# Kernel optimization log

Measured on AMD Instinct MI355X. Metric: run time of the kernel, lower is better.

The kernel has to match this reference:

```python
import jax, jax.numpy as jnp
import numpy as np

D_MODEL = 1024
D_K = 64
HEADS = 16


def setup_inputs() -> dict:
    key = jax.random.key(0)
    k = jax.random.split(key, 7)
    b, s = 4, 2048
    scale = 1.0 / np.sqrt(D_MODEL)
    return {
        "input_Q": jax.random.normal(k[0], (b, s, D_MODEL), jnp.float32),
        "input_K": jax.random.normal(k[1], (b, s, D_MODEL), jnp.float32),
        "input_V": jax.random.normal(k[2], (b, s, D_MODEL), jnp.float32),
        "W_Q": jax.random.normal(k[3], (D_MODEL, D_K * HEADS), jnp.float32) * scale,
        "W_K": jax.random.normal(k[4], (D_MODEL, D_K * HEADS), jnp.float32) * scale,
        "W_V": jax.random.normal(k[5], (D_MODEL, D_K * HEADS), jnp.float32) * scale,
        "W_O": jax.random.normal(k[6], (D_K * HEADS, D_MODEL), jnp.float32) * scale,
    }


def reference(input_Q, input_K, input_V, W_Q, W_K, W_V, W_O):
    b, s, _ = input_Q.shape
    # project and split heads: [b, s, h*d] -> [b, h, s, d]
    def split_heads(x):
        return x.reshape(b, -1, HEADS, D_K).transpose(0, 2, 1, 3)

    Q = split_heads(input_Q @ W_Q)
    K = split_heads(input_K @ W_K)
    V = split_heads(input_V @ W_V)

    scores = jnp.einsum("bhsd,bhtd->bhst", Q, K) / np.sqrt(D_K)  # [b,h,s,s]
    attn = jax.nn.softmax(scores, axis=-1)
    value = jnp.einsum("bhst,bhtd->bhsd", attn, V)  # [b,h,s,d]
    value = value.transpose(0, 2, 1, 3).reshape(b, s, HEADS * D_K)
    return value @ W_O
```

## Files before the change

kernel.cpp:

```cpp
#include <hip/hip_runtime.h>
#include <stdint.h>

#define DM 1024
#define HD 64
#define NH 16
#define SEQ 2048
#define NB 4

typedef __bf16 bf16x8 __attribute__((ext_vector_type(8)));
typedef __bf16 bf16x4 __attribute__((ext_vector_type(4)));
typedef float f32x4 __attribute__((ext_vector_type(4)));

#define EXP2F(x) __builtin_amdgcn_exp2f(x)

__device__ __forceinline__ float bf2f(uint16_t b) {
    uint32_t u = ((uint32_t)b) << 16;
    float f;
    __builtin_memcpy(&f, &u, 4);
    return f;
}
__device__ __forceinline__ uint16_t f2bf(float f) {
    uint32_t u;
    __builtin_memcpy(&u, &f, 4);
    u += 0x7fffu + ((u >> 16) & 1u);
    return (uint16_t)(u >> 16);
}

__device__ __forceinline__ void gll16(const void* g, void* l) {
    __builtin_amdgcn_global_load_lds(
        (const __attribute__((address_space(1))) void*)g,
        (__attribute__((address_space(3))) void*)l, 16, 0, 0);
}

__global__ __launch_bounds__(256) void cvt_f32_bf16(const float* __restrict__ in,
                                                    uint16_t* __restrict__ out) {
    const size_t i = (size_t)blockIdx.x * 256 + threadIdx.x;
    const float4* p = (const float4*)in + i * 2;
    const float4 a = p[0], b = p[1];
    uint16_t o[8] = {f2bf(a.x), f2bf(a.y), f2bf(a.z), f2bf(a.w),
                     f2bf(b.x), f2bf(b.y), f2bf(b.z), f2bf(b.w)};
    __builtin_memcpy(out + i * 8, o, 16);
}

__global__ void transpose_cvt4(const float* __restrict__ w0,
                               const float* __restrict__ w1,
                               const float* __restrict__ w2,
                               const float* __restrict__ w3,
                               uint16_t* __restrict__ o0,
                               uint16_t* __restrict__ o1,
                               uint16_t* __restrict__ o2,
                               uint16_t* __restrict__ o3) {
    __shared__ uint16_t t[32][33];
    const float* in;
    uint16_t* out;
    switch (blockIdx.z) {
        case 0: in = w0; out = o0; break;
        case 1: in = w1; out = o1; break;
        case 2: in = w2; out = o2; break;
        default: in = w3; out = o3; break;
    }
    const int bx = blockIdx.x * 32, by = blockIdx.y * 32;
    const int tx = threadIdx.x, ty = threadIdx.y;
#pragma unroll
    for (int i = ty; i < 32; i += 8)
        t[i][tx] = f2bf(in[(size_t)(by + i) * DM + bx + tx]);
    __syncthreads();
#pragma unroll
    for (int i = ty; i < 32; i += 8)
        out[(size_t)(bx + i) * DM + by + tx] = t[tx][i];
}

__global__ void transpose_bf16(const uint16_t* __restrict__ in,
                               uint16_t* __restrict__ out, int R, int C) {
    __shared__ uint16_t t[32][33];
    const int bx = blockIdx.x * 32, by = blockIdx.y * 32;
    const size_t zo = (size_t)blockIdx.z * R * C;
    in += zo; out += zo;
    const int tx = threadIdx.x, ty = threadIdx.y;
#pragma unroll
    for (int i = ty; i < 32; i += 8)
        t[i][tx] = in[(size_t)(by + i) * C + bx + tx];
    __syncthreads();
#pragma unroll
    for (int i = ty; i < 32; i += 8)
        out[(size_t)(bx + i) * R + by + tx] = t[tx][i];
}

template <typename OT>
__global__ __launch_bounds__(256) void gemm_bf16(
    const uint16_t* __restrict__ A, const uint16_t* __restrict__ Bt,
    OT* __restrict__ C, int M, int N, int K) {
    __shared__ uint16_t As[2][128 * 64];
    __shared__ uint16_t Bs[2][128 * 64];
    const int tid = threadIdx.x;
    const int wave = tid >> 6, lane = tid & 63;
    const int g = lane >> 4, l15 = lane & 15;
    const int m0 = blockIdx.y * 128, n0 = blockIdx.x * 128;
    const int wr = wave >> 1, wc = wave & 1;

    size_t aglob[4], bglob[4];
    int ldsOff[4];
#pragma unroll
    for (int i = 0; i < 4; i++) {
        const int c = wave * 4 + i;
        const int o = (c * 64 + lane) * 16;
        const int row = o >> 7, off = o & 127;
        const int soff = off ^ ((row & 7) << 4);
        aglob[i] = ((size_t)(m0 + row) * K << 1) + soff;
        bglob[i] = ((size_t)(n0 + row) * K << 1) + soff;
        ldsOff[i] = c * 1024;
    }

    f32x4 acc[4][4];
    const f32x4 z4 = {0.f, 0.f, 0.f, 0.f};
#pragma unroll
    for (int i = 0; i < 4; i++)
#pragma unroll
        for (int j = 0; j < 4; j++) acc[i][j] = z4;

#pragma unroll
    for (int i = 0; i < 4; i++) {
        gll16((const char*)A + aglob[i], (char*)As[0] + ldsOff[i]);
        gll16((const char*)Bt + bglob[i], (char*)Bs[0] + ldsOff[i]);
    }
#pragma unroll
    for (int i = 0; i < 4; i++) {
        gll16((const char*)A + aglob[i] + 128, (char*)As[1] + ldsOff[i]);
        gll16((const char*)Bt + bglob[i] + 128, (char*)Bs[1] + ldsOff[i]);
    }

    const int steps = K >> 6;
    for (int s = 0; s < steps; s++) {
        if (s + 1 < steps)
            asm volatile("s_waitcnt vmcnt(8)" ::: "memory");
        else
            asm volatile("s_waitcnt vmcnt(0)" ::: "memory");
        __builtin_amdgcn_sched_barrier(0);
        __builtin_amdgcn_s_barrier();
        __builtin_amdgcn_sched_barrier(0);

        const uint16_t* as = As[s & 1];
        const uint16_t* bs = Bs[s & 1];
#pragma unroll
        for (int ks = 0; ks < 2; ks++) {
            bf16x8 a[4], b[4];
#pragma unroll
            for (int mi = 0; mi < 4; mi++) {
                const int row = wr * 64 + mi * 16 + l15;
                a[mi] = *(const bf16x8*)((const char*)as + row * 128 +
                                         ((ks * 64 + g * 16) ^ ((row & 7) << 4)));
            }
#pragma unroll
            for (int ni = 0; ni < 4; ni++) {
                const int row = wc * 64 + ni * 16 + l15;
                b[ni] = *(const bf16x8*)((const char*)bs + row * 128 +
                                         ((ks * 64 + g * 16) ^ ((row & 7) << 4)));
            }
#pragma unroll
            for (int mi = 0; mi < 4; mi++)
#pragma unroll
                for (int ni = 0; ni < 4; ni++)
                    acc[mi][ni] = __builtin_amdgcn_mfma_f32_16x16x32_bf16(
                        a[mi], b[ni], acc[mi][ni], 0, 0, 0);
        }

        __builtin_amdgcn_sched_barrier(0);
        __builtin_amdgcn_s_barrier();
        __builtin_amdgcn_sched_barrier(0);

        if (s + 2 < steps) {
            const size_t kb = ((size_t)(s + 2) << 7);
#pragma unroll
            for (int i = 0; i < 4; i++) {
                gll16((const char*)A + aglob[i] + kb, (char*)As[s & 1] + ldsOff[i]);
                gll16((const char*)Bt + bglob[i] + kb, (char*)Bs[s & 1] + ldsOff[i]);
            }
        }
    }

#pragma unroll
    for (int mi = 0; mi < 4; mi++)
#pragma unroll
        for (int ni = 0; ni < 4; ni++) {
            const int row = m0 + wr * 64 + mi * 16 + g * 4;
            const int col = n0 + wc * 64 + ni * 16 + l15;
#pragma unroll
            for (int r = 0; r < 4; r++) {
                if constexpr (sizeof(OT) == 4)
                    C[(size_t)(row + r) * N + col] = acc[mi][ni][r];
                else
                    C[(size_t)(row + r) * N + col] = f2bf(acc[mi][ni][r]);
            }
        }
}

__global__ __launch_bounds__(256, 2) void attn_fwd(
    const uint16_t* __restrict__ Q, const uint16_t* __restrict__ Kb,
    const uint16_t* __restrict__ Vt, uint16_t* __restrict__ AO) {
    __shared__ uint16_t smem[6 * 4096];
    const int tid = threadIdx.x;
    const int wave = tid >> 6, lane = tid & 63;
    const int g = lane >> 4, l15 = lane & 15;
    const int qt = blockIdx.x, h = blockIdx.y, b = blockIdx.z;
    const int q0 = qt * 256 + wave * 64;
    const int NT = SEQ / 64;
    const float SM_BIAS = 12.0f;

    uint16_t* const KsBase = smem;
    uint16_t* const VsBase = smem + 3 * 4096;

    size_t kglob[2], vglob[2];
    int ldsOff[2];
#pragma unroll
    for (int i = 0; i < 2; i++) {
        const int c = wave * 2 + i;
        const int r3 = (lane >> 3) & 7;
        const int soff = ((lane & 7) << 4) ^ (r3 << 4);
        const int kappa = (((c >> 1) & 1) << 5) | ((c & 1) << 4) |
                          (((lane >> 5) & 1) << 3) | (((c >> 2) & 1) << 2) |
                          (r3 & 3);
        kglob[i] = (((size_t)(b * SEQ + kappa) * DM + h * HD) << 1) + soff;
        vglob[i] = (((size_t)(b * DM + h * HD + c * 8 + r3) * SEQ) << 1) + soff;
        ldsOff[i] = c * 1024;
    }

    const float QSCALE = 0.125f * 1.44269504088896f;
    bf16x8 qf[4][2];
#pragma unroll
    for (int qi = 0; qi < 4; qi++)
#pragma unroll
        for (int ks = 0; ks < 2; ks++) {
            const uint16_t* src = Q + (size_t)(b * SEQ + q0 + qi * 16 + l15) * DM +
                                  h * HD + ks * 32 + g * 8;
            uint16_t tmp[8], ov[8];
            __builtin_memcpy(tmp, src, 16);
#pragma unroll
            for (int j = 0; j < 8; j++) ov[j] = f2bf(bf2f(tmp[j]) * QSCALE);
            __builtin_memcpy(&qf[qi][ks], ov, 16);
        }

    f32x4 accO[4][4];
    const f32x4 z4 = {0.f, 0.f, 0.f, 0.f};
#pragma unroll
    for (int i = 0; i < 4; i++)
#pragma unroll
        for (int j = 0; j < 4; j++) accO[i][j] = z4;
    float l_run[4] = {0.f, 0.f, 0.f, 0.f};

#pragma unroll
    for (int i = 0; i < 2; i++) {
        gll16((const char*)Kb + kglob[i], (char*)KsBase + ldsOff[i]);
        gll16((const char*)Vt + vglob[i], (char*)VsBase + ldsOff[i]);
    }
    {
        const size_t kadv = (size_t)(64 * DM * 2);
        const size_t vadv = (size_t)(64 * 2);
#pragma unroll
        for (int i = 0; i < 2; i++) {
            gll16((const char*)Kb + kglob[i] + kadv, (char*)KsBase + 8192 + ldsOff[i]);
            gll16((const char*)Vt + vglob[i] + vadv, (char*)VsBase + 8192 + ldsOff[i]);
        }
    }

    int cur = 0;
    for (int kt = 0; kt < NT; kt++) {
        if (kt + 1 < NT)
            asm volatile("s_waitcnt vmcnt(4)" ::: "memory");
        else
            asm volatile("s_waitcnt vmcnt(0)" ::: "memory");
        __builtin_amdgcn_sched_barrier(0);
        __builtin_amdgcn_s_barrier();
        __builtin_amdgcn_sched_barrier(0);

        if (kt + 2 < NT) {
            const int nb = (cur == 0) ? 2 : cur - 1;
            const size_t kadv = (size_t)(kt + 2) * (64 * DM * 2);
            const size_t vadv = (size_t)(kt + 2) * (64 * 2);
#pragma unroll
            for (int i = 0; i < 2; i++) {
                gll16((const char*)Kb + kglob[i] + kadv,
                      (char*)KsBase + nb * 8192 + ldsOff[i]);
                gll16((const char*)Vt + vglob[i] + vadv,
                      (char*)VsBase + nb * 8192 + ldsOff[i]);
            }
        }
        const uint16_t* ksrc = KsBase + cur * 4096;
        const uint16_t* vsrc = VsBase + cur * 4096;
        cur = (cur == 2) ? 0 : cur + 1;

        f32x4 sf[4][4];
        const f32x4 bias4 = {-SM_BIAS, -SM_BIAS, -SM_BIAS, -SM_BIAS};
#pragma unroll
        for (int kf = 0; kf < 4; kf++)
#pragma unroll
            for (int qi = 0; qi < 4; qi++) sf[kf][qi] = bias4;
        __builtin_amdgcn_s_setprio(1);
#pragma unroll
        for (int ks = 0; ks < 2; ks++)
#pragma unroll
            for (int kf = 0; kf < 4; kf++) {
                const int row = kf * 16 + l15;
                bf16x8 a = *(const bf16x8*)((const char*)ksrc + row * 128 +
                                            ((ks * 64 + g * 16) ^ ((row & 7) << 4)));
#pragma unroll
                for (int qi = 0; qi < 4; qi++)
                    sf[kf][qi] = __builtin_amdgcn_mfma_f32_16x16x32_bf16(
                        a, qf[qi][ks], sf[kf][qi], 0, 0, 0);
            }
        __builtin_amdgcn_s_setprio(0);

        bf16x8 pa[4][2];
#pragma unroll
        for (int qi = 0; qi < 4; qi++) {
            float ls = 0.f;
#pragma unroll
            for (int ks = 0; ks < 2; ks++) {
                bf16x8 v;
#pragma unroll
                for (int j = 0; j < 4; j++) {
                    const float p = EXP2F(sf[ks][qi][j]);
                    ls += p;
                    v[j] = (__bf16)p;
                }
#pragma unroll
                for (int j = 0; j < 4; j++) {
                    const float p = EXP2F(sf[ks + 2][qi][j]);
                    ls += p;
                    v[4 + j] = (__bf16)p;
                }
                pa[qi][ks] = v;
            }
            l_run[qi] += ls;
        }

        __builtin_amdgcn_s_setprio(1);
#pragma unroll
        for (int ks = 0; ks < 2; ks++)
#pragma unroll
            for (int nf = 0; nf < 4; nf++) {
                const int row = nf * 16 + l15;
                bf16x8 av = *(const bf16x8*)((const char*)vsrc + row * 128 +
                                             ((ks * 64 + g * 16) ^ ((row & 7) << 4)));
#pragma unroll
                for (int qi = 0; qi < 4; qi++)
                    accO[qi][nf] = __builtin_amdgcn_mfma_f32_16x16x32_bf16(
                        av, pa[qi][ks], accO[qi][nf], 0, 0, 0);
            }
        __builtin_amdgcn_s_setprio(0);
    }

    __syncthreads();

#pragma unroll
    for (int qi = 0; qi < 4; qi++) {
        l_run[qi] += __shfl_xor(l_run[qi], 16);
        l_run[qi] += __shfl_xor(l_run[qi], 32);
        l_run[qi] = 1.f / l_run[qi];
    }

    uint16_t* bw = smem + wave * 4096;
#pragma unroll
    for (int qi = 0; qi < 4; qi++) {
        const int q = qi * 16 + l15;
        const int swz = (q & 7) << 4;
#pragma unroll
        for (int nf = 0; nf < 4; nf++) {
            bf16x4 ov;
            ov[0] = (__bf16)(accO[qi][nf][0] * l_run[qi]);
            ov[1] = (__bf16)(accO[qi][nf][1] * l_run[qi]);
            ov[2] = (__bf16)(accO[qi][nf][2] * l_run[qi]);
            ov[3] = (__bf16)(accO[qi][nf][3] * l_run[qi]);
            const int off = (q * 128 + nf * 32 + g * 8) ^ swz;
            __builtin_memcpy((char*)bw + off, &ov, 8);
        }
    }
    __syncthreads();
#pragma unroll
    for (int qq = 0; qq < 2; qq++) {
        const int q = qq * 32 + (lane >> 1), part = lane & 1;
        const int swz = (q & 7) << 4;
        const size_t orow = ((size_t)(b * SEQ + q0 + q) * DM) + h * HD + part * 32;
#pragma unroll
        for (int t = 0; t < 4; t++) {
            bf16x8 ov;
            __builtin_memcpy(&ov,
                             (const char*)bw + ((q * 128 + part * 64 + t * 16) ^ swz),
                             16);
            __builtin_memcpy(&AO[orow + t * 8], &ov, 16);
        }
    }
}

extern "C" void kernel_launch(void* const* d_in, const int* in_sizes, int n_in,
                              void* d_out, int out_size, void* d_ws, size_t ws_size,
                              hipStream_t stream) {
    const float* xq = (const float*)d_in[0];
    const float* xk = (const float*)d_in[1];
    const float* xv = (const float*)d_in[2];
    const float* wq = (const float*)d_in[3];
    const float* wk = (const float*)d_in[4];
    const float* wv = (const float*)d_in[5];
    const float* wo = (const float*)d_in[6];
    float* out = (float*)d_out;
    uint16_t* ws = (uint16_t*)d_ws;

    const size_t SZ = (size_t)NB * SEQ * DM;
    const size_t WSZ = (size_t)DM * DM;
    uint16_t* bufA = ws;
    uint16_t* Qb = ws + SZ;
    uint16_t* Kbuf = ws + 2 * SZ;
    uint16_t* Vb = ws + 3 * SZ;
    uint16_t* WqT = ws + 4 * SZ;
    uint16_t* WkT = WqT + WSZ;
    uint16_t* WvT = WkT + WSZ;
    uint16_t* WoT = WvT + WSZ;

    const dim3 tb(32, 8);
    transpose_cvt4<<<dim3(32, 32, 4), tb, 0, stream>>>(wq, wk, wv, wo,
                                                       WqT, WkT, WvT, WoT);

    const int cvtBlocks = (int)(SZ / (256 * 8));
    const dim3 gg(DM / 128, NB * SEQ / 128);

    cvt_f32_bf16<<<cvtBlocks, 256, 0, stream>>>(xq, bufA);
    gemm_bf16<uint16_t><<<gg, 256, 0, stream>>>(bufA, WqT, Qb, NB * SEQ, DM, DM);

    cvt_f32_bf16<<<cvtBlocks, 256, 0, stream>>>(xk, bufA);
    gemm_bf16<uint16_t><<<gg, 256, 0, stream>>>(bufA, WkT, Kbuf, NB * SEQ, DM, DM);

    cvt_f32_bf16<<<cvtBlocks, 256, 0, stream>>>(xv, bufA);
    gemm_bf16<uint16_t><<<gg, 256, 0, stream>>>(bufA, WvT, Vb, NB * SEQ, DM, DM);

    transpose_bf16<<<dim3(DM / 32, SEQ / 32, NB), tb, 0, stream>>>(Vb, bufA, SEQ, DM);

    attn_fwd<<<dim3(SEQ / 256, NH, NB), 256, 0, stream>>>(Qb, Kbuf, bufA, Vb);

    gemm_bf16<float><<<gg, 256, 0, stream>>>(Vb, WoT, out, NB * SEQ, DM, DM);
}
```

Measured before the change: 219.3 us.

## Fuse fp32-to-bf16 conversion, QKV projections and V transpose into one GEMM kernel

Replaces three separate conversion kernels, three projection GEMMs and the V transpose with a single batched gemm_qkv launch over z=3. The kernel loads fp32 activations directly into registers, converts them to bf16 while writing to LDS, and for V writes the output already transposed through an LDS staging buffer. The intent is to remove the intermediate bf16 activation round trips, the separate transpose pass and several launches. In exchange the A operand now goes through a register-prefetch path instead of async global-to-LDS loads, which could expose more latency per step.

Measured after the change: 226.9 us. 1.03x slower.

```diff
diff --git a/kernel.cpp b/kernel.cpp
--- a/kernel.cpp
+++ b/kernel.cpp
@@ -30,16 +30,6 @@
     __builtin_amdgcn_global_load_lds(
         (const __attribute__((address_space(1))) void*)g,
         (__attribute__((address_space(3))) void*)l, 16, 0, 0);
-}
-
-__global__ __launch_bounds__(256) void cvt_f32_bf16(const float* __restrict__ in,
-                                                    uint16_t* __restrict__ out) {
-    const size_t i = (size_t)blockIdx.x * 256 + threadIdx.x;
-    const float4* p = (const float4*)in + i * 2;
-    const float4 a = p[0], b = p[1];
-    uint16_t o[8] = {f2bf(a.x), f2bf(a.y), f2bf(a.z), f2bf(a.w),
-                     f2bf(b.x), f2bf(b.y), f2bf(b.z), f2bf(b.w)};
-    __builtin_memcpy(out + i * 8, o, 16);
 }
 
 __global__ void transpose_cvt4(const float* __restrict__ w0,
@@ -70,20 +60,166 @@
         out[(size_t)(bx + i) * DM + by + tx] = t[tx][i];
 }
 
-__global__ void transpose_bf16(const uint16_t* __restrict__ in,
-                               uint16_t* __restrict__ out, int R, int C) {
-    __shared__ uint16_t t[32][33];
-    const int bx = blockIdx.x * 32, by = blockIdx.y * 32;
-    const size_t zo = (size_t)blockIdx.z * R * C;
-    in += zo; out += zo;
-    const int tx = threadIdx.x, ty = threadIdx.y;
-#pragma unroll
-    for (int i = ty; i < 32; i += 8)
-        t[i][tx] = in[(size_t)(by + i) * C + bx + tx];
-    __syncthreads();
-#pragma unroll
-    for (int i = ty; i < 32; i += 8)
-        out[(size_t)(bx + i) * R + by + tx] = t[tx][i];
+__global__ __launch_bounds__(256, 2) void gemm_qkv(
+    const float* __restrict__ xq, const float* __restrict__ xk,
+    const float* __restrict__ xv, const uint16_t* __restrict__ wqt,
+    const uint16_t* __restrict__ wkt, const uint16_t* __restrict__ wvt,
+    uint16_t* __restrict__ outq, uint16_t* __restrict__ outk,
+    uint16_t* __restrict__ outvt) {
+    __shared__ uint16_t smem[32768];
+    const float* A;
+    const uint16_t* Bt;
+    uint16_t* C;
+    bool trans;
+    if (blockIdx.z == 0) { A = xq; Bt = wqt; C = outq; trans = false; }
+    else if (blockIdx.z == 1) { A = xk; Bt = wkt; C = outk; trans = false; }
+    else { A = xv; Bt = wvt; C = outvt; trans = true; }
+    const int K = DM, N = DM;
+
+    const int tid = threadIdx.x;
+    const int wave = tid >> 6, lane = tid & 63;
+    const int g = lane >> 4, l15 = lane & 15;
+    const int m0 = blockIdx.y * 128, n0 = blockIdx.x * 128;
+    const int wr = wave >> 1, wc = wave & 1;
+    char* const smb = (char*)smem;
+
+    size_t aoff[4], bglob[4];
+    int adst[4];
+#pragma unroll
+    for (int i = 0; i < 4; i++) {
+        const int c = wave * 4 + i;
+        const int arow = c * 8 + (lane >> 3);
+        aoff[i] = ((size_t)(m0 + arow) * K + (lane & 7) * 8) << 2;
+        adst[i] = c * 1024 + (lane >> 3) * 128 +
+                  (((lane & 7) << 4) ^ ((lane >> 3) << 4));
+        const int o = (c * 64 + lane) * 16;
+        const int brow = o >> 7, boff = o & 127;
+        bglob[i] = ((size_t)(n0 + brow) * K << 1) + (boff ^ ((brow & 7) << 4));
+    }
+
+    f32x4 acc[4][4];
+    const f32x4 z4 = {0.f, 0.f, 0.f, 0.f};
+#pragma unroll
+    for (int i = 0; i < 4; i++)
+#pragma unroll
+        for (int j = 0; j < 4; j++) acc[i][j] = z4;
+
+    float4 apf[4][2];
+#pragma unroll
+    for (int i = 0; i < 4; i++)
+        gll16((const char*)Bt + bglob[i], smb + 32768 + (wave * 4 + i) * 1024);
+#pragma unroll
+    for (int i = 0; i < 4; i++) {
+        apf[i][0] = *(const float4*)((const char*)A + aoff[i]);
+        apf[i][1] = *(const float4*)((const char*)A + aoff[i] + 16);
+    }
+    __builtin_amdgcn_sched_barrier(0);
+
+    const int steps = K >> 6;
+    for (int s = 0; s < steps; s++) {
+        asm volatile("s_waitcnt vmcnt(0)" ::: "memory");
+        __builtin_amdgcn_sched_barrier(0);
+        __builtin_amdgcn_s_barrier();
+        __builtin_amdgcn_sched_barrier(0);
+
+        const int abase = (s & 1) * 16384;
+#pragma unroll
+        for (int i = 0; i < 4; i++) {
+            bf16x8 v;
+            v[0] = (__bf16)apf[i][0].x;
+            v[1] = (__bf16)apf[i][0].y;
+            v[2] = (__bf16)apf[i][0].z;
+            v[3] = (__bf16)apf[i][0].w;
+            v[4] = (__bf16)apf[i][1].x;
+            v[5] = (__bf16)apf[i][1].y;
+            v[6] = (__bf16)apf[i][1].z;
+            v[7] = (__bf16)apf[i][1].w;
+            *(bf16x8*)(smb + abase + adst[i]) = v;
+        }
+        if (s + 1 < steps) {
+            const size_t ka = (size_t)(s + 1) << 8;
+#pragma unroll
+            for (int i = 0; i < 4; i++) {
+                apf[i][0] = *(const float4*)((const char*)A + aoff[i] + ka);
+                apf[i][1] = *(const float4*)((const char*)A + aoff[i] + ka + 16);
+            }
+            const size_t kb = (size_t)(s + 1) << 7;
+            const int bbuf = 32768 + ((s + 1) & 1) * 16384;
+#pragma unroll
+            for (int i = 0; i < 4; i++)
+                gll16((const char*)Bt + bglob[i] + kb,
+                      smb + bbuf + (wave * 4 + i) * 1024);
+        }
+        asm volatile("s_waitcnt lgkmcnt(0)" ::: "memory");
+        __builtin_amdgcn_sched_barrier(0);
+        __builtin_amdgcn_s_barrier();
+        __builtin_amdgcn_sched_barrier(0);
+
+        const char* as_ = smb + abase;
+        const char* bs_ = smb + 32768 + (s & 1) * 16384;
+#pragma unroll
+        for (int ks = 0; ks < 2; ks++) {
+            bf16x8 a[4], b[4];
+#pragma unroll
+            for (int mi = 0; mi < 4; mi++) {
+                const int row = wr * 64 + mi * 16 + l15;
+                a[mi] = *(const bf16x8*)(as_ + row * 128 +
+                                         ((ks * 64 + g * 16) ^ ((row & 7) << 4)));
+            }
+#pragma unroll
+            for (int ni = 0; ni < 4; ni++) {
+                const int row = wc * 64 + ni * 16 + l15;
+                b[ni] = *(const bf16x8*)(bs_ + row * 128 +
+                                         ((ks * 64 + g * 16) ^ ((row & 7) << 4)));
+            }
+#pragma unroll
+            for (int mi = 0; mi < 4; mi++)
+#pragma unroll
+                for (int ni = 0; ni < 4; ni++)
+                    acc[mi][ni] = __builtin_amdgcn_mfma_f32_16x16x32_bf16(
+                        a[mi], b[ni], acc[mi][ni], 0, 0, 0);
+        }
+    }
+
+    if (!trans) {
+#pragma unroll
+        for (int mi = 0; mi < 4; mi++)
+#pragma unroll
+            for (int ni = 0; ni < 4; ni++) {
+                const int row = m0 + wr * 64 + mi * 16 + g * 4;
+                const int col = n0 + wc * 64 + ni * 16 + l15;
+#pragma unroll
+                for (int r = 0; r < 4; r++)
+                    C[(size_t)(row + r) * N + col] = f2bf(acc[mi][ni][r]);
+            }
+    } else {
+        __syncthreads();
+#pragma unroll
+        for (int mi = 0; mi < 4; mi++)
+#pragma unroll
+            for (int ni = 0; ni < 4; ni++) {
+                const int col = wc * 64 + ni * 16 + l15;
+                const int row = wr * 64 + mi * 16 + g * 4;
+                bf16x4 v;
+                v[0] = (__bf16)acc[mi][ni][0];
+                v[1] = (__bf16)acc[mi][ni][1];
+                v[2] = (__bf16)acc[mi][ni][2];
+                v[3] = (__bf16)acc[mi][ni][3];
+                __builtin_memcpy(smb + col * 272 + row * 2, &v, 8);
+            }
+        __syncthreads();
+        const int b0 = m0 >> 11, s0 = m0 & 2047;
+        const int c = tid >> 1, half = tid & 1;
+#pragma unroll
+        for (int t = 0; t < 8; t++) {
+            bf16x8 v;
+            __builtin_memcpy(&v, smb + c * 272 + half * 128 + t * 16, 16);
+            __builtin_memcpy((char*)C +
+                                 (((size_t)b0 * DM + n0 + c) * SEQ + s0 +
+                                  half * 64 + t * 8) * 2,
+                             &v, 16);
+        }
+    }
 }
 
 template <typename OT>
@@ -406,10 +542,10 @@
 
     const size_t SZ = (size_t)NB * SEQ * DM;
     const size_t WSZ = (size_t)DM * DM;
-    uint16_t* bufA = ws;
+    uint16_t* Vt = ws;
     uint16_t* Qb = ws + SZ;
     uint16_t* Kbuf = ws + 2 * SZ;
-    uint16_t* Vb = ws + 3 * SZ;
+    uint16_t* AO = ws + 3 * SZ;
     uint16_t* WqT = ws + 4 * SZ;
     uint16_t* WkT = WqT + WSZ;
     uint16_t* WvT = WkT + WSZ;
@@ -419,21 +555,11 @@
     transpose_cvt4<<<dim3(32, 32, 4), tb, 0, stream>>>(wq, wk, wv, wo,
                                                        WqT, WkT, WvT, WoT);
 
-    const int cvtBlocks = (int)(SZ / (256 * 8));
-    const dim3 gg(DM / 128, NB * SEQ / 128);
-
-    cvt_f32_bf16<<<cvtBlocks, 256, 0, stream>>>(xq, bufA);
-    gemm_bf16<uint16_t><<<gg, 256, 0, stream>>>(bufA, WqT, Qb, NB * SEQ, DM, DM);
-
-    cvt_f32_bf16<<<cvtBlocks, 256, 0, stream>>>(xk, bufA);
-    gemm_bf16<uint16_t><<<gg, 256, 0, stream>>>(bufA, WkT, Kbuf, NB * SEQ, DM, DM);
-
-    cvt_f32_bf16<<<cvtBlocks, 256, 0, stream>>>(xv, bufA);
-    gemm_bf16<uint16_t><<<gg, 256, 0, stream>>>(bufA, WvT, Vb, NB * SEQ, DM, DM);
-
-    transpose_bf16<<<dim3(DM / 32, SEQ / 32, NB), tb, 0, stream>>>(Vb, bufA, SEQ, DM);
-
-    attn_fwd<<<dim3(SEQ / 256, NH, NB), 256, 0, stream>>>(Qb, Kbuf, bufA, Vb);
-
-    gemm_bf16<float><<<gg, 256, 0, stream>>>(Vb, WoT, out, NB * SEQ, DM, DM);
-}
+    gemm_qkv<<<dim3(DM / 128, NB * SEQ / 128, 3), 256, 0, stream>>>(
+        xq, xk, xv, WqT, WkT, WvT, Qb, Kbuf, Vt);
+
+    attn_fwd<<<dim3(SEQ / 256, NH, NB), 256, 0, stream>>>(Qb, Kbuf, Vt, AO);
+
+    gemm_bf16<float><<<dim3(DM / 128, NB * SEQ / 128), 256, 0, stream>>>(
+        AO, WoT, out, NB * SEQ, DM, DM);
+}
```
